# Performance work log

Measured on AMD Instinct MI355X. Metric: run time of the kernel, lower is better.

The kernel has to match this reference:

```python
import jax, jax.numpy as jnp
import numpy as np

D = 1024       # embedding_dim
H = 16         # num_attention_heads
B = 2
S = 2048       # seq_len == context_len


def setup_inputs() -> dict:
    key = jax.random.key(0)
    k1, k2, k3 = jax.random.split(key, 3)
    X = jax.random.normal(k1, (B, S, D), dtype=jnp.float32)
    W_qkv = jax.random.normal(k2, (D, 3 * D), dtype=jnp.float32) * 0.02
    b_qkv = jnp.zeros((3 * D,), dtype=jnp.float32)
    W_out = jax.random.normal(k3, (D, D), dtype=jnp.float32) * 0.02
    b_out = jnp.zeros((D,), dtype=jnp.float32)
    return {"X": X, "W_qkv": W_qkv, "b_qkv": b_qkv, "W_out": W_out, "b_out": b_out}


def reference(X, W_qkv, b_qkv, W_out, b_out):
    b, s, d = X.shape
    hd = d // H
    # fused QKV projection (GPT-2 Conv1D == x @ W + b)
    qkv = X @ W_qkv + b_qkv                       # [b, s, 3d]
    q, k, v = jnp.split(qkv, 3, axis=2)
    # [b, h, s, hd]
    q = q.reshape(b, s, H, hd).transpose(0, 2, 1, 3)
    k = k.reshape(b, s, H, hd).transpose(0, 2, 1, 3)
    v = v.reshape(b, s, H, hd).transpose(0, 2, 1, 3)
    # NOTE: source scales by rsqrt(embedding_dim), not head_dim
    scale = 1.0 / jnp.sqrt(jnp.float32(d))
    scores = jnp.einsum("bhqd,bhkd->bhqk", q, k) * scale
    causal = jnp.tril(jnp.ones((s, s), dtype=bool))
    scores = jnp.where(causal[None, None], scores, -jnp.inf)
    # attention_dropout applied pre-softmax in source; identity at eval (p used here = 0)
    probs = jax.nn.softmax(scores, axis=-1)
    attn = jnp.einsum("bhqk,bhkd->bhqd", probs, v)
    attn = attn.transpose(0, 2, 1, 3).reshape(b, s, d)
    out = attn @ W_out + b_out                    # outwards proj; dropout eval = identity
    return out
```

## Files before the change

kernel.cpp:

```cpp
#include <hip/hip_runtime.h>

#define S_LEN 2048
#define DIM   1024
#define NHEAD 16
#define HDIM  64
#define Q_PRESCALE 0.045084220027780106f

typedef __attribute__((ext_vector_type(8))) short  short8;
typedef __attribute__((ext_vector_type(4))) float  floatx4;
typedef __attribute__((ext_vector_type(4))) unsigned short ushort4v;
typedef __attribute__((ext_vector_type(4))) unsigned int uintx4;

__device__ inline unsigned short f2bf(float f) {
  unsigned v = __builtin_bit_cast(unsigned, f);
  v += 0x7FFFu + ((v >> 16) & 1u);
  return (unsigned short)(v >> 16);
}

__device__ inline unsigned cvt_pk_bf16(float a, float b) {
  unsigned r;
  asm("v_cvt_pk_bf16_f32 %0, %1, %2" : "=v"(r) : "v"(a), "v"(b));
  return r;
}

__device__ inline void async16(const unsigned short* g, unsigned short* l) {
  __builtin_amdgcn_global_load_lds(
      (const __attribute__((address_space(1))) unsigned int*)g,
      (__attribute__((address_space(3))) unsigned int*)l, 16, 0, 0);
}

__global__ __launch_bounds__(256) void prep_kernel(
    const float* __restrict__ X, const float* __restrict__ Wqkv,
    const float* __restrict__ Wout, unsigned short* __restrict__ Xb,
    unsigned short* __restrict__ Wqkvt, unsigned short* __restrict__ Woutt) {
  const int j = blockIdx.x, t = threadIdx.x;
  if (j >= 4096) {
    int i = ((j - 4096) * 256 + t) * 8;
    float4 a = *(const float4*)&X[i];
    float4 b = *(const float4*)&X[i + 4];
    short8 o;
    o[0] = (short)f2bf(a.x); o[1] = (short)f2bf(a.y);
    o[2] = (short)f2bf(a.z); o[3] = (short)f2bf(a.w);
    o[4] = (short)f2bf(b.x); o[5] = (short)f2bf(b.y);
    o[6] = (short)f2bf(b.z); o[7] = (short)f2bf(b.w);
    *(short8*)&Xb[i] = o;
    return;
  }
  __shared__ unsigned short tile[32][33];
  const float* in; unsigned short* out; int N, tn, tk;
  if (j < 3072) { in = Wqkv; out = Wqkvt; N = 3072; tn = j % 96; tk = j / 96; }
  else { int u = j - 3072; in = Wout; out = Woutt; N = 1024; tn = u & 31; tk = u >> 5; }
  const int n0 = tn * 32, k0 = tk * 32;
  const int tx = t & 31, ty = t >> 5;
#pragma unroll
  for (int i = 0; i < 32; i += 8)
    tile[ty + i][tx] = f2bf(in[(size_t)(k0 + ty + i) * N + n0 + tx]);
  __syncthreads();
#pragma unroll
  for (int i = 0; i < 32; i += 8)
    out[(size_t)(n0 + ty + i) * 1024 + k0 + tx] = tile[tx][ty + i];
}

#define GEMM128_BODY(APTR, BPTR)                                                   \
  __shared__ __align__(16) unsigned short As[128][64];                             \
  __shared__ __align__(16) unsigned short Bs[128][64];                             \
  const int m0 = blockIdx.y * 128, n0 = blockIdx.x * 128;                          \
  const int t = threadIdx.x, lane = t & 63, wave = t >> 6;                         \
  const int quad = lane >> 4, l16 = lane & 15;                                     \
  const int wm = (wave >> 1) * 64, wn = (wave & 1) * 64;                           \
  const int lr = lane >> 3, lc = lane & 7, sc8 = (lc ^ lr) * 8;                    \
  const int sw = l16 & 7;                                                          \
  const int pA0 = (quad ^ sw) * 8, pA1 = ((4 + quad) ^ sw) * 8;                    \
  floatx4 acc[4][4];                                                               \
  _Pragma("unroll") for (int mi = 0; mi < 4; mi++)                                 \
      _Pragma("unroll") for (int ni = 0; ni < 4; ni++)                             \
          acc[mi][ni] = (floatx4){0.f, 0.f, 0.f, 0.f};                             \
  for (int k0 = 0; k0 < DIM; k0 += 64) {                                           \
    _Pragma("unroll") for (int i = 0; i < 4; i++) {                                \
      int rb = wave * 32 + i * 8;                                                  \
      async16(&APTR[(size_t)(m0 + rb + lr) * DIM + k0 + sc8], &As[rb][0]);         \
      async16(&BPTR[(size_t)(n0 + rb + lr) * DIM + k0 + sc8], &Bs[rb][0]);         \
    }                                                                              \
    __syncthreads();                                                               \
    short8 a0[4], a1[4];                                                           \
    _Pragma("unroll") for (int mi = 0; mi < 4; mi++) {                             \
      int row = wm + mi * 16 + l16;                                                \
      a0[mi] = *(const short8*)&As[row][pA0];                                      \
      a1[mi] = *(const short8*)&As[row][pA1];                                      \
    }                                                                              \
    _Pragma("unroll") for (int ni = 0; ni < 4; ni++) {                             \
      int row = wn + ni * 16 + l16;                                                \
      short8 b0 = *(const short8*)&Bs[row][pA0];                                   \
      short8 b1 = *(const short8*)&Bs[row][pA1];                                   \
      _Pragma("unroll") for (int mi = 0; mi < 4; mi++) {                           \
        acc[mi][ni] = __builtin_amdgcn_mfma_f32_16x16x32_bf16(a0[mi], b0, acc[mi][ni], 0, 0, 0); \
        acc[mi][ni] = __builtin_amdgcn_mfma_f32_16x16x32_bf16(a1[mi], b1, acc[mi][ni], 0, 0, 0); \
      }                                                                            \
    }                                                                              \
    __syncthreads();                                                               \
  }

__global__ __launch_bounds__(256) void gemm_qkv128(
    const unsigned short* __restrict__ Xb,
    const unsigned short* __restrict__ Wt,
    const float* __restrict__ bias,
    unsigned short* __restrict__ Qg,
    unsigned short* __restrict__ Kg,
    unsigned short* __restrict__ Vgt) {
  GEMM128_BODY(Xb, Wt)
  const int section = n0 >> 10;
  const int head = ((n0 + wn) >> 6) & 15;
#pragma unroll
  for (int mi = 0; mi < 4; mi++) {
    int mg = m0 + wm + mi * 16 + quad * 4;
    int bb = mg >> 11, sb = mg & 2047;
    size_t y = (size_t)bb * NHEAD + head;
    if (section == 2) {
#pragma unroll
      for (int ni = 0; ni < 4; ni++) {
        int hdi = ni * 16 + l16;
        float bv = bias[n0 + wn + hdi];
        ushort4v o;
#pragma unroll
        for (int r = 0; r < 4; r++) o[r] = f2bf(acc[mi][ni][r] + bv);
        *(ushort4v*)&Vgt[(y * HDIM + hdi) * S_LEN + sb] = o;
      }
    } else if (section == 0) {
#pragma unroll
      for (int ni = 0; ni < 4; ni++) {
        int hdi = ni * 16 + l16;
        float bv = bias[n0 + wn + hdi];
#pragma unroll
        for (int r = 0; r < 4; r++)
          Qg[(y * S_LEN + sb + r) * HDIM + hdi] = f2bf((acc[mi][ni][r] + bv) * Q_PRESCALE);
      }
    } else {
#pragma unroll
      for (int ni = 0; ni < 4; ni++) {
        int hdi = ni * 16 + l16;
        float bv = bias[n0 + wn + hdi];
#pragma unroll
        for (int r = 0; r < 4; r++)
          Kg[(y * S_LEN + sb + r) * HDIM + hdi] = f2bf(acc[mi][ni][r] + bv);
      }
    }
  }
}

__global__ __launch_bounds__(128) void gemm_out64(
    const unsigned short* __restrict__ A,
    const unsigned short* __restrict__ Wt,
    const float* __restrict__ bias,
    float* __restrict__ outp) {
  __shared__ __align__(16) unsigned short As[64][64];
  __shared__ __align__(16) unsigned short Bs[128][64];
  const int m0 = blockIdx.y * 64, n0 = blockIdx.x * 128;
  const int t = threadIdx.x, lane = t & 63, wave = t >> 6;
  const int quad = lane >> 4, l16 = lane & 15;
  const int wn = wave * 64;
  const int lr = lane >> 3, lc = lane & 7, sc8 = (lc ^ lr) * 8;
  const int sw = l16 & 7;
  const int pA0 = (quad ^ sw) * 8, pA1 = ((4 + quad) ^ sw) * 8;
  floatx4 acc[4][4];
#pragma unroll
  for (int mi = 0; mi < 4; mi++)
#pragma unroll
    for (int ni = 0; ni < 4; ni++) acc[mi][ni] = (floatx4){0.f, 0.f, 0.f, 0.f};

  for (int k0 = 0; k0 < DIM; k0 += 64) {
#pragma unroll
    for (int i = 0; i < 4; i++) {
      int rb = wave * 32 + i * 8;
      async16(&A[(size_t)(m0 + rb + lr) * DIM + k0 + sc8], &As[rb][0]);
    }
#pragma unroll
    for (int i = 0; i < 8; i++) {
      int rb = wave * 64 + i * 8;
      async16(&Wt[(size_t)(n0 + rb + lr) * DIM + k0 + sc8], &Bs[rb][0]);
    }
    __syncthreads();
    short8 a0[4], a1[4];
#pragma unroll
    for (int mi = 0; mi < 4; mi++) {
      int row = mi * 16 + l16;
      a0[mi] = *(const short8*)&As[row][pA0];
      a1[mi] = *(const short8*)&As[row][pA1];
    }
#pragma unroll
    for (int ni = 0; ni < 4; ni++) {
      int row = wn + ni * 16 + l16;
      short8 b0 = *(const short8*)&Bs[row][pA0];
      short8 b1 = *(const short8*)&Bs[row][pA1];
#pragma unroll
      for (int mi = 0; mi < 4; mi++) {
        acc[mi][ni] = __builtin_amdgcn_mfma_f32_16x16x32_bf16(a0[mi], b0, acc[mi][ni], 0, 0, 0);
        acc[mi][ni] = __builtin_amdgcn_mfma_f32_16x16x32_bf16(a1[mi], b1, acc[mi][ni], 0, 0, 0);
      }
    }
    __syncthreads();
  }
#pragma unroll
  for (int ni = 0; ni < 4; ni++) {
    int n = n0 + wn + ni * 16 + l16;
    float bv = bias[n];
#pragma unroll
    for (int mi = 0; mi < 4; mi++) {
      int mg = m0 + mi * 16 + quad * 4;
#pragma unroll
      for (int r = 0; r < 4; r++)
        outp[(size_t)(mg + r) * DIM + n] = acc[mi][ni][r] + bv;
    }
  }
}

__global__ __launch_bounds__(256) void gemm_qkv_kernel(
    const float* __restrict__ X,
    const unsigned short* __restrict__ Wt,
    const float* __restrict__ bias,
    unsigned short* __restrict__ Qg,
    unsigned short* __restrict__ Kg,
    unsigned short* __restrict__ Vgt,
    int g0, int G) {
  __shared__ __align__(16) unsigned short As[64][72];
  __shared__ __align__(16) unsigned short Bs[64][72];
  const int tn = blockIdx.x;
  const int section = tn / G, within = tn % G;
  const int n0 = section * 1024 + (g0 + within) * 64;
  const int m0 = blockIdx.y * 64;
  const int t = threadIdx.x, lane = t & 63, wave = t >> 6;
  const int quad = lane >> 4, l16 = lane & 15;

  floatx4 acc[4];
#pragma unroll
  for (int i = 0; i < 4; i++) acc[i] = (floatx4){0.f, 0.f, 0.f, 0.f};

  for (int k0 = 0; k0 < DIM; k0 += 64) {
#pragma unroll
    for (int i = 0; i < 2; i++) {
      int v = t + i * 256;
      int row = v >> 3, cc = (v & 7) * 8;
      float4 f0 = *(const float4*)&X[(size_t)(m0 + row) * DIM + k0 + cc];
      float4 f1 = *(const float4*)&X[(size_t)(m0 + row) * DIM + k0 + cc + 4];
      short8 o;
      o[0] = (short)f2bf(f0.x); o[1] = (short)f2bf(f0.y);
      o[2] = (short)f2bf(f0.z); o[3] = (short)f2bf(f0.w);
      o[4] = (short)f2bf(f1.x); o[5] = (short)f2bf(f1.y);
      o[6] = (short)f2bf(f1.z); o[7] = (short)f2bf(f1.w);
      *(short8*)&As[row][cc] = o;
      *(short8*)&Bs[row][cc] = *(const short8*)&Wt[(size_t)(n0 + row) * DIM + k0 + cc];
    }
    __syncthreads();
    short8 a0 = *(const short8*)&As[wave * 16 + l16][quad * 8];
    short8 a1 = *(const short8*)&As[wave * 16 + l16][32 + quad * 8];
#pragma unroll
    for (int nt = 0; nt < 4; nt++) {
      short8 b0 = *(const short8*)&Bs[nt * 16 + l16][quad * 8];
      short8 b1 = *(const short8*)&Bs[nt * 16 + l16][32 + quad * 8];
      acc[nt] = __builtin_amdgcn_mfma_f32_16x16x32_bf16(a0, b0, acc[nt], 0, 0, 0);
      acc[nt] = __builtin_amdgcn_mfma_f32_16x16x32_bf16(a1, b1, acc[nt], 0, 0, 0);
    }
    __syncthreads();
  }

  const int mbase = m0 + wave * 16 + quad * 4;
  const int b = mbase >> 11, sbase = mbase & 2047;
  const int y = b * G + within;
  if (section == 2) {
#pragma unroll
    for (int nt = 0; nt < 4; nt++) {
      int hdi = nt * 16 + l16;
      float bv = bias[n0 + hdi];
      ushort4v o;
#pragma unroll
      for (int r = 0; r < 4; r++) o[r] = f2bf(acc[nt][r] + bv);
      *(ushort4v*)&Vgt[((size_t)y * HDIM + hdi) * S_LEN + sbase] = o;
    }
  } else if (section == 0) {
#pragma unroll
    for (int nt = 0; nt < 4; nt++) {
      int hdi = nt * 16 + l16;
      float bv = bias[n0 + hdi];
#pragma unroll
      for (int r = 0; r < 4; r++)
        Qg[((size_t)y * S_LEN + sbase + r) * HDIM + hdi] =
            f2bf((acc[nt][r] + bv) * Q_PRESCALE);
    }
  } else {
#pragma unroll
    for (int nt = 0; nt < 4; nt++) {
      int hdi = nt * 16 + l16;
      float bv = bias[n0 + hdi];
#pragma unroll
      for (int r = 0; r < 4; r++)
        Kg[((size_t)y * S_LEN + sbase + r) * HDIM + hdi] = f2bf(acc[nt][r] + bv);
    }
  }
}

__global__ __launch_bounds__(256) void attn_kernel(
    const unsigned short* __restrict__ Qg,
    const unsigned short* __restrict__ Kg,
    const unsigned short* __restrict__ Vgt,
    unsigned short* __restrict__ attnB) {
  __shared__ __align__(16) unsigned short Ks[2][64][64];
  __shared__ __align__(16) unsigned short Vs[2][64][64];

  const int y = blockIdx.x;
  const int b = y >> 4, h = y & 15;
  const int qt = 31 - blockIdx.y;
  const int q0 = qt * 64;
  const int nT = qt + 1;
  const int t = threadIdx.x;
  const int lane = t & 63, wave = t >> 6;
  const int quad = lane >> 4, l16 = lane & 15;
  const int lr = lane >> 3, lc = lane & 7;
  const int sc8 = (lc ^ lr) * 8;
  const int sw = l16 & 7;
  const int p0 = (quad ^ sw) * 8, p1 = ((4 + quad) ^ sw) * 8;

  const unsigned short* Qh = Qg + (size_t)y * S_LEN * HDIM;
  const unsigned short* Kh = Kg + (size_t)y * S_LEN * HDIM;
  const unsigned short* Vh = Vgt + (size_t)y * HDIM * S_LEN;

  const unsigned ov = (l16 == 0) ? 0x3F803F80u : 0u;
  const uintx4 ou = {ov, ov, ov, ov};
  const short8 ones = __builtin_bit_cast(short8, ou);

  const int srcA = (((2 * quad) & 3) << 4) | l16;
  const int srcB = (((2 * quad + 1) & 3) << 4) | l16;
  const bool hiq = (quad & 2) != 0;

  short8 aq0, aq1;
  {
    const unsigned short* qp = &Qh[(size_t)(q0 + wave * 16 + l16) * HDIM];
    aq0 = *(const short8*)&qp[quad * 8];
    aq1 = *(const short8*)&qp[32 + quad * 8];
  }

  floatx4 o_acc[5];
#pragma unroll
  for (int dt = 0; dt < 5; dt++) o_acc[dt] = (floatx4){0.f, 0.f, 0.f, 0.f};

  {
    int rb = wave * 16;
#pragma unroll
    for (int i = 0; i < 2; i++) {
      async16(&Kh[(size_t)(rb + i * 8 + lr) * HDIM + sc8], &Ks[0][rb + i * 8][0]);
      async16(&Vh[(size_t)(rb + i * 8 + lr) * S_LEN + sc8], &Vs[0][rb + i * 8][0]);
    }
  }

  for (int tt = 0; tt < nT; tt++) {
    const int j0 = tt * 64;
    const int buf = tt & 1;
    __syncthreads();
    if (tt + 1 < nT) {
      int j1 = j0 + 64, nb = 1 - buf;
      int rb = wave * 16;
#pragma unroll
      for (int i = 0; i < 2; i++) {
        async16(&Kh[(size_t)(j1 + rb + i * 8 + lr) * HDIM + sc8], &Ks[nb][rb + i * 8][0]);
        async16(&Vh[(size_t)(rb + i * 8 + lr) * S_LEN + j1 + sc8], &Vs[nb][rb + i * 8][0]);
      }
    }

    floatx4 sc[4];
#pragma unroll
    for (int nt = 0; nt < 4; nt++) {
      short8 kb0 = *(const short8*)&Ks[buf][nt * 16 + l16][p0];
      short8 kb1 = *(const short8*)&Ks[buf][nt * 16 + l16][p1];
      sc[nt] = (floatx4){0.f, 0.f, 0.f, 0.f};
      sc[nt] = __builtin_amdgcn_mfma_f32_16x16x32_bf16(kb0, aq0, sc[nt], 0, 0, 0);
      sc[nt] = __builtin_amdgcn_mfma_f32_16x16x32_bf16(kb1, aq1, sc[nt], 0, 0, 0);
    }

    float p[4][4];
#pragma unroll
    for (int nt = 0; nt < 4; nt++)
#pragma unroll
      for (int r = 0; r < 4; r++)
        p[nt][r] = exp2f(sc[nt][r]);
    if (j0 == q0) {
      const int ql = wave * 16 + l16;
#pragma unroll
      for (int nt = 0; nt < 4; nt++)
#pragma unroll
        for (int r = 0; r < 4; r++)
          if (nt * 16 + quad * 4 + r > ql) p[nt][r] = 0.f;
    }

    unsigned pk00 = cvt_pk_bf16(p[0][0], p[0][1]), pk01 = cvt_pk_bf16(p[0][2], p[0][3]);
    unsigned pk10 = cvt_pk_bf16(p[1][0], p[1][1]), pk11 = cvt_pk_bf16(p[1][2], p[1][3]);
    unsigned pk20 = cvt_pk_bf16(p[2][0], p[2][1]), pk21 = cvt_pk_bf16(p[2][2], p[2][3]);
    unsigned pk30 = cvt_pk_bf16(p[3][0], p[3][1]), pk31 = cvt_pk_bf16(p[3][2], p[3][3]);

    unsigned w0a = __shfl(pk00, srcA), w0b = __shfl(pk10, srcA);
    unsigned w1a = __shfl(pk01, srcA), w1b = __shfl(pk11, srcA);
    unsigned w2a = __shfl(pk00, srcB), w2b = __shfl(pk10, srcB);
    unsigned w3a = __shfl(pk01, srcB), w3b = __shfl(pk11, srcB);
    uintx4 u0 = {hiq ? w0b : w0a, hiq ? w1b : w1a, hiq ? w2b : w2a, hiq ? w3b : w3a};
    short8 ap0 = __builtin_bit_cast(short8, u0);

    unsigned w4a = __shfl(pk20, srcA), w4b = __shfl(pk30, srcA);
    unsigned w5a = __shfl(pk21, srcA), w5b = __shfl(pk31, srcA);
    unsigned w6a = __shfl(pk20, srcB), w6b = __shfl(pk30, srcB);
    unsigned w7a = __shfl(pk21, srcB), w7b = __shfl(pk31, srcB);
    uintx4 u1 = {hiq ? w4b : w4a, hiq ? w5b : w5a, hiq ? w6b : w6a, hiq ? w7b : w7a};
    short8 ap1 = __builtin_bit_cast(short8, u1);

#pragma unroll
    for (int dt = 0; dt < 5; dt++) {
      short8 vb0 = (dt < 4) ? *(const short8*)&Vs[buf][dt * 16 + l16][p0] : ones;
      short8 vb1 = (dt < 4) ? *(const short8*)&Vs[buf][dt * 16 + l16][p1] : ones;
      o_acc[dt] = __builtin_amdgcn_mfma_f32_16x16x32_bf16(ap0, vb0, o_acc[dt], 0, 0, 0);
      o_acc[dt] = __builtin_amdgcn_mfma_f32_16x16x32_bf16(ap1, vb1, o_acc[dt], 0, 0, 0);
    }
  }

  float linv[4];
#pragma unroll
  for (int r = 0; r < 4; r++)
    linv[r] = 1.0f / __shfl(o_acc[4][r], quad << 4);
#pragma unroll
  for (int dt = 0; dt < 4; dt++)
#pragma unroll
    for (int r = 0; r < 4; r++) {
      int qg = q0 + wave * 16 + quad * 4 + r;
      attnB[(size_t)(b * S_LEN + qg) * DIM + h * HDIM + dt * 16 + l16] =
          f2bf(o_acc[dt][r] * linv[r]);
    }
}

extern "C" void kernel_launch(void* const* d_in, const int* in_sizes, int n_in,
                              void* d_out, int out_size, void* d_ws, size_t ws_size,
                              hipStream_t stream) {
  const float* X    = (const float*)d_in[0];
  const float* Wqkv = (const float*)d_in[1];
  const float* bqkv = (const float*)d_in[2];
  const float* Wout = (const float*)d_in[3];
  const float* bout = (const float*)d_in[4];
  float* outp = (float*)d_out;

  unsigned short* Wqkvt = (unsigned short*)d_ws;
  unsigned short* Woutt = Wqkvt + (size_t)3145728;
  unsigned short* attnB = Woutt + (size_t)1048576;
  unsigned short* Qg    = attnB + (size_t)4194304;
  unsigned short* Kg    = Qg + (size_t)4194304;
  unsigned short* Vgt   = Kg + (size_t)4194304;
  unsigned short* Xb    = Vgt + (size_t)4194304;

  const bool bigWs = ws_size >= (size_t)48 * 1024 * 1024;

  if (bigWs) {
    prep_kernel<<<6144, 256, 0, stream>>>(X, Wqkv, Wout, Xb, Wqkvt, Woutt);
    gemm_qkv128<<<dim3(24, 32), 256, 0, stream>>>(Xb, Wqkvt, bqkv, Qg, Kg, Vgt);
  } else {
    prep_kernel<<<4096, 256, 0, stream>>>(X, Wqkv, Wout, nullptr, Wqkvt, Woutt);
    gemm_qkv_kernel<<<dim3(48, 64), 256, 0, stream>>>(
        X, Wqkvt, bqkv, Qg, Kg, Vgt, 0, 16);
  }
  attn_kernel<<<dim3(32, 32), 256, 0, stream>>>(Qg, Kg, Vgt, attnB);
  gemm_out64<<<dim3(8, 64), 128, 0, stream>>>(attnB, Woutt, bout, outp);
}
```

Measured before the change: 191.6 us.

## Use permlane swaps for P transpose and XCD-aware block remapping

Replaces the 16 ds_bpermute-based shuffles that rearrange softmax probabilities into MFMA A-operand layout with permlane32_swap and permlane16_swap register-lane exchanges, which avoid the LDS crossbar path. Also remaps block indices in the two GEMMs and the attention kernel so that consecutive logical tiles land on the same XCD (stride-8 round-robin), aiming to improve L2 reuse of shared A/B or K/V tiles. The remap assumes the grid size is divisible by 8 and the attention grid is 32x32. The lane permutation must exactly match the previous shuffle pattern or results will be wrong.

```diff
diff --git a/kernel.cpp b/kernel.cpp
--- a/kernel.cpp
+++ b/kernel.cpp
@@ -21,6 +21,10 @@
   unsigned r;
   asm("v_cvt_pk_bf16_f32 %0, %1, %2" : "=v"(r) : "v"(a), "v"(b));
   return r;
+}
+
+__device__ inline void permlane16_swap_rw(unsigned &a, unsigned &b) {
+  asm volatile("v_permlane16_swap_b32 %0, %1" : "+v"(a), "+v"(b));
 }
 
 __device__ inline void async16(const unsigned short* g, unsigned short* l) {
@@ -64,7 +68,10 @@
 #define GEMM128_BODY(APTR, BPTR)                                                   \
   __shared__ __align__(16) unsigned short As[128][64];                             \
   __shared__ __align__(16) unsigned short Bs[128][64];                             \
-  const int m0 = blockIdx.y * 128, n0 = blockIdx.x * 128;                          \
+  const int _L = blockIdx.x + gridDim.x * blockIdx.y;                              \
+  const int _cpx = (gridDim.x * gridDim.y) >> 3;                                   \
+  const int _s = (_L & 7) * _cpx + (_L >> 3);                                      \
+  const int m0 = (_s / gridDim.x) * 128, n0 = (_s % gridDim.x) * 128;              \
   const int t = threadIdx.x, lane = t & 63, wave = t >> 6;                         \
   const int quad = lane >> 4, l16 = lane & 15;                                     \
   const int wm = (wave >> 1) * 64, wn = (wave & 1) * 64;                           \
@@ -154,7 +161,10 @@
     float* __restrict__ outp) {
   __shared__ __align__(16) unsigned short As[64][64];
   __shared__ __align__(16) unsigned short Bs[128][64];
-  const int m0 = blockIdx.y * 64, n0 = blockIdx.x * 128;
+  const int _L = blockIdx.x + gridDim.x * blockIdx.y;
+  const int _cpx = (gridDim.x * gridDim.y) >> 3;
+  const int _s = (_L & 7) * _cpx + (_L >> 3);
+  const int m0 = (_s / gridDim.x) * 64, n0 = (_s % gridDim.x) * 128;
   const int t = threadIdx.x, lane = t & 63, wave = t >> 6;
   const int quad = lane >> 4, l16 = lane & 15;
   const int wn = wave * 64;
@@ -305,9 +315,11 @@
   __shared__ __align__(16) unsigned short Ks[2][64][64];
   __shared__ __align__(16) unsigned short Vs[2][64][64];
 
-  const int y = blockIdx.x;
+  const int L = blockIdx.x + 32 * blockIdx.y;
+  const int s = (L & 7) * 128 + (L >> 3);
+  const int y = s >> 5;
   const int b = y >> 4, h = y & 15;
-  const int qt = 31 - blockIdx.y;
+  const int qt = 31 - (s & 31);
   const int q0 = qt * 64;
   const int nT = qt + 1;
   const int t = threadIdx.x;
@@ -326,10 +338,6 @@
   const uintx4 ou = {ov, ov, ov, ov};
   const short8 ones = __builtin_bit_cast(short8, ou);
 
-  const int srcA = (((2 * quad) & 3) << 4) | l16;
-  const int srcB = (((2 * quad + 1) & 3) << 4) | l16;
-  const bool hiq = (quad & 2) != 0;
-
   short8 aq0, aq1;
   {
     const unsigned short* qp = &Qh[(size_t)(q0 + wave * 16 + l16) * HDIM];
@@ -394,18 +402,21 @@
     unsigned pk20 = cvt_pk_bf16(p[2][0], p[2][1]), pk21 = cvt_pk_bf16(p[2][2], p[2][3]);
     unsigned pk30 = cvt_pk_bf16(p[3][0], p[3][1]), pk31 = cvt_pk_bf16(p[3][2], p[3][3]);
 
-    unsigned w0a = __shfl(pk00, srcA), w0b = __shfl(pk10, srcA);
-    unsigned w1a = __shfl(pk01, srcA), w1b = __shfl(pk11, srcA);
-    unsigned w2a = __shfl(pk00, srcB), w2b = __shfl(pk10, srcB);
-    unsigned w3a = __shfl(pk01, srcB), w3b = __shfl(pk11, srcB);
-    uintx4 u0 = {hiq ? w0b : w0a, hiq ? w1b : w1a, hiq ? w2b : w2a, hiq ? w3b : w3a};
+    auto sa0 = __builtin_amdgcn_permlane32_swap(pk00, pk10, false, false);
+    auto sa1 = __builtin_amdgcn_permlane32_swap(pk01, pk11, false, false);
+    auto sb0 = __builtin_amdgcn_permlane32_swap(pk20, pk30, false, false);
+    auto sb1 = __builtin_amdgcn_permlane32_swap(pk21, pk31, false, false);
+    unsigned xa0 = (unsigned)sa0[0], ya0 = (unsigned)sa0[1];
+    unsigned xa1 = (unsigned)sa1[0], ya1 = (unsigned)sa1[1];
+    unsigned xb0 = (unsigned)sb0[0], yb0 = (unsigned)sb0[1];
+    unsigned xb1 = (unsigned)sb1[0], yb1 = (unsigned)sb1[1];
+    permlane16_swap_rw(xa0, ya0);
+    permlane16_swap_rw(xa1, ya1);
+    permlane16_swap_rw(xb0, yb0);
+    permlane16_swap_rw(xb1, yb1);
+    uintx4 u0 = {xa0, xa1, ya0, ya1};
     short8 ap0 = __builtin_bit_cast(short8, u0);
-
-    unsigned w4a = __shfl(pk20, srcA), w4b = __shfl(pk30, srcA);
-    unsigned w5a = __shfl(pk21, srcA), w5b = __shfl(pk31, srcA);
-    unsigned w6a = __shfl(pk20, srcB), w6b = __shfl(pk30, srcB);
-    unsigned w7a = __shfl(pk21, srcB), w7b = __shfl(pk31, srcB);
-    uintx4 u1 = {hiq ? w4b : w4a, hiq ? w5b : w5a, hiq ? w6b : w6a, hiq ? w7b : w7a};
+    uintx4 u1 = {xb0, xb1, yb0, yb1};
     short8 ap1 = __builtin_bit_cast(short8, u1);
 
 #pragma unroll
```

After: 207.9 us. 1.08x slower.
